# Kernel tuning notes

Hardware: AMD Instinct MI355X
Metric: run time of the kernel (lower is better)

The kernel has to match this reference:

```python
import jax, jax.numpy as jnp
import numpy as np

ANCHOR = 12.0      # anchor (d,h,w) size used for parametrization
NMS_IOU = 0.25     # suppression threshold
TOPK = 2048        # pre-NMS candidate cap (= stop_after), fixed for jit


def setup_inputs() -> dict:
    key = jax.random.key(0)
    k1, k2 = jax.random.split(key)
    bboxes = jax.random.normal(k1, (2, 6, 64, 96, 96), dtype=jnp.float32)
    scores = jax.random.normal(k2, (2, 64, 96, 96), dtype=jnp.float32)
    return {"bboxes": bboxes, "scores": scores}


def _deparametrize(bboxes):
    # bboxes: (B, 6, D, H, W), parametrized as in Ren et al. 2017
    D, H, W = bboxes.shape[2:]
    axes = [jnp.arange(s, dtype=bboxes.dtype) + 0.5 for s in (D, H, W)]
    zyx = jnp.stack(jnp.meshgrid(*axes, indexing='ij'))        # (3, D, H, W)
    abs_zyx = bboxes[:, :3] * ANCHOR + zyx[None]               # center coords
    abs_dhw = jnp.exp(bboxes[:, 3:]) * ANCHOR                  # sizes
    return jnp.concatenate([abs_zyx, abs_dhw], axis=1)


def _pairwise_iou(b1, b2):
    # b1: (N,6), b2: (M,6) with (z,y,x,d,h,w)
    c1, s1 = b1[:, :3], b1[:, 3:]
    c2, s2 = b2[:, :3], b2[:, 3:]
    lo = jnp.maximum((c1 - s1 / 2)[:, None, :], (c2 - s2 / 2)[None, :, :])
    hi = jnp.minimum((c1 + s1 / 2)[:, None, :], (c2 + s2 / 2)[None, :, :])
    inter = jnp.clip(hi - lo, 0).prod(-1)                      # (N, M)
    union = s1.prod(-1)[:, None] + s2.prod(-1)[None, :] - inter
    return inter / union


def _nms_one(boxes_flat, scores_flat):
    # boxes_flat: (P, 6), scores_flat: (P,)
    scores_top, idx = jax.lax.top_k(scores_flat, TOPK)
    boxes_top = boxes_flat[idx]                                # (K, 6)
    ious = _pairwise_iou(boxes_top, boxes_top)                 # (K, K)
    ar = jnp.arange(TOPK)

    def body(keep, i):
        # suppress lower-scored boxes overlapping a kept box i
        suppress = (ious[i] > NMS_IOU) & (ar > i) & keep[i]
        return keep & ~suppress, None

    keep, _ = jax.lax.scan(body, jnp.ones(TOPK, dtype=bool), ar)
    out = jnp.concatenate([scores_top[:, None], boxes_top], axis=1)  # (K, 7)
    return jnp.where(keep[:, None], out, 0.0)


def reference(bboxes, scores):
    abs_boxes = _deparametrize(bboxes)                         # (B, 6, D, H, W)
    B = bboxes.shape[0]
    boxes_flat = abs_boxes.reshape(B, 6, -1).transpose(0, 2, 1)  # (B, P, 6)
    scores_flat = scores.reshape(B, -1)                          # (B, P)
    # (B, TOPK, 7): column 0 = score, columns 1:7 = (z,y,x,d,h,w); suppressed rows zeroed
    return jax.vmap(_nms_one)(boxes_flat, scores_flat)
```

## Files before the change

### kernel.cpp

```cpp
#include <hip/hip_runtime.h>
#include <math.h>

typedef unsigned int U32;
typedef unsigned long long U64;

constexpr int N_SP   = 64 * 96 * 96;
constexpr int NBATCH = 2;
constexpr int K_TOP  = 2048;
constexpr int NBINS  = 8192;
constexpr int CAP    = 8192;
constexpr int CAPB   = 128;
constexpr float ANCHOR_F = 12.0f;
constexpr float NMS_IOU_F = 0.25f;

constexpr size_t OFF_HIST = 0;
constexpr size_t OFF_CNT  = OFF_HIST + 2 * NBINS * 4;
constexpr size_t OFF_THR  = OFF_CNT + 256;
constexpr size_t OFF_RANK = OFF_THR + 256;
constexpr size_t OFF_CAND = OFF_RANK + 2 * CAP * 4;
constexpr size_t OFF_BOX  = OFF_CAND + 2 * CAP * 8;
constexpr size_t OFF_MASK = OFF_BOX + 2 * 14 * K_TOP * 4;
constexpr size_t OFF_DIAG = OFF_MASK + 2 * K_TOP * 64 * 4;
constexpr size_t OFF_BCNT = OFF_DIAG + 2 * K_TOP * 4;
constexpr size_t OFF_BKT  = OFF_BCNT + 512;

__device__ __forceinline__ U32 mono_of(float f) {
  U32 u = __float_as_uint(f);
  return (u & 0x80000000u) ? ~u : (u | 0x80000000u);
}
__device__ __forceinline__ float un_mono(U32 m) {
  U32 u = (m & 0x80000000u) ? (m ^ 0x80000000u) : ~m;
  return __uint_as_float(u);
}

__global__ void __launch_bounds__(256) k_zero(U32* hist, U32* rank, U32* cnt,
                                              U32* bcnt) {
  int g = blockIdx.x * 256 + threadIdx.x;
  hist[g] = 0;
  rank[g] = 0;
  if (g < NBATCH) cnt[g] = 0;
  if (g < 2 * 64) bcnt[g] = 0;
}

__global__ void __launch_bounds__(256) k_hist(const float* __restrict__ scores,
                                              U32* __restrict__ hist) {
  int b = blockIdx.y;
  const float4* s4 = (const float4*)(scores + (size_t)b * N_SP)
                     + (size_t)blockIdx.x * 2048 + threadIdx.x;
  float4 v[8];
#pragma unroll
  for (int e = 0; e < 8; ++e) v[e] = s4[e * 256];
  __shared__ U32 lh[NBINS];
  for (int k = threadIdx.x; k < NBINS; k += 256) lh[k] = 0;
  __syncthreads();
#pragma unroll
  for (int e = 0; e < 8; ++e) {
    atomicAdd(&lh[mono_of(v[e].x) >> 19], 1u);
    atomicAdd(&lh[mono_of(v[e].y) >> 19], 1u);
    atomicAdd(&lh[mono_of(v[e].z) >> 19], 1u);
    atomicAdd(&lh[mono_of(v[e].w) >> 19], 1u);
  }
  __syncthreads();
  U32* gh = hist + (size_t)b * NBINS;
  for (int k = threadIdx.x; k < NBINS; k += 256) {
    U32 c = lh[k];
    if (c) atomicAdd(&gh[k], c);
  }
}

__global__ void __launch_bounds__(256) k_thresh(const U32* __restrict__ hist,
                                                U32* __restrict__ thr) {
  int b = blockIdx.x;
  const U32* h = hist + (size_t)b * NBINS;
  __shared__ U32 part[256];
  int t = threadIdx.x;
  int base = NBINS - 32 * (t + 1);
  U32 s = 0;
  for (int k = 0; k < 32; ++k) s += h[base + k];
  part[t] = s;
  __syncthreads();
  if (t == 0) {
    U32 cum = 0, bin = 0;
    for (int c = 0; c < 256; ++c) {
      U32 p = part[c];
      if (cum + p >= (U32)K_TOP) {
        int hb = NBINS - 32 * c - 1;
        for (int k = 0; k < 32; ++k) {
          cum += h[hb - k];
          if (cum >= (U32)K_TOP) { bin = (U32)(hb - k); break; }
        }
        break;
      }
      cum += p;
    }
    thr[b] = bin;
  }
}

__global__ void __launch_bounds__(256) k_collect(const float* __restrict__ scores,
                                                 const U32* __restrict__ thr,
                                                 U32* __restrict__ cnt,
                                                 U64* __restrict__ cand) {
  int b = blockIdx.y;
  U32 tb = thr[b];
  const float4* s4 = (const float4*)(scores + (size_t)b * N_SP)
                     + (size_t)blockIdx.x * 1024 + threadIdx.x;
  float4 v[4];
#pragma unroll
  for (int e = 0; e < 4; ++e) v[e] = s4[e * 256];
  __shared__ U64 lbuf[4096];
  __shared__ U32 lcnt, lbase;
  if (threadIdx.x == 0) lcnt = 0;
  __syncthreads();
#pragma unroll
  for (int e = 0; e < 4; ++e) {
    U32 i0 = (blockIdx.x * 1024 + e * 256 + threadIdx.x) * 4;
    float vv[4] = {v[e].x, v[e].y, v[e].z, v[e].w};
#pragma unroll
    for (int c = 0; c < 4; ++c) {
      U32 m = mono_of(vv[c]);
      if ((m >> 19) >= tb) {
        U32 p = atomicAdd(&lcnt, 1u);
        lbuf[p] = ((U64)m << 32) | (U32)(~(i0 + c));
      }
    }
  }
  __syncthreads();
  if (threadIdx.x == 0 && lcnt) lbase = atomicAdd(&cnt[b], lcnt);
  __syncthreads();
  U32 n = lcnt;
  if (n == 0) return;
  U32 base = lbase;
  U64* cb = cand + (size_t)b * CAP;
  for (U32 k = threadIdx.x; k < n; k += 256) {
    U32 pos = base + k;
    if (pos < (U32)CAP) cb[pos] = lbuf[k];
  }
}

__global__ void __launch_bounds__(256) k_count(const U64* __restrict__ cand,
                                               const U32* __restrict__ cnt,
                                               U32* __restrict__ rank) {
  int b = blockIdx.y;
  U32 C = cnt[b]; if (C > (U32)CAP) C = CAP;
  U32 g = blockIdx.x * 256 + threadIdx.x;
  U32 t = g & (CAP - 1);
  U32 sgm = g >> 13;
  if (t >= C) return;
  const U64* cb = cand + (size_t)b * CAP;
  U64 key = cb[t];
  U32 segLen = (C + 7) >> 3;
  U32 j0 = sgm * segLen;
  U32 j1 = j0 + segLen; if (j1 > C) j1 = C;
  U32 c = 0;
  for (U32 j = j0; j < j1; ++j) c += (cb[j] > key) ? 1u : 0u;
  if (c) atomicAdd(&rank[(size_t)b * CAP + t], c);
}

#pragma clang fp contract(off)

__global__ void __launch_bounds__(256) k_gather(const float* __restrict__ bboxes,
                                                const U64* __restrict__ cand,
                                                const U32* __restrict__ cnt,
                                                const U32* __restrict__ rank,
                                                float* __restrict__ box) {
  int b = blockIdx.y;
  U32 C = cnt[b]; if (C > (U32)CAP) C = CAP;
  U32 t = blockIdx.x * 256 + threadIdx.x;
  if (t >= C) return;
  U32 r = rank[(size_t)b * CAP + t];
  if (r >= (U32)K_TOP) return;
  U64 key = cand[(size_t)b * CAP + t];
  U32 idx = ~(U32)(key & 0xFFFFFFFFull);
  float sc = un_mono((U32)(key >> 32));
  int d = idx / 9216;
  int rem = idx - d * 9216;
  int h = rem / 96;
  int w = rem - h * 96;
  const float* src = bboxes + (size_t)b * 6 * N_SP + idx;
  float r0 = src[0];
  float r1 = src[(size_t)N_SP];
  float r2 = src[(size_t)2 * N_SP];
  float r3 = src[(size_t)3 * N_SP];
  float r4 = src[(size_t)4 * N_SP];
  float r5 = src[(size_t)5 * N_SP];
  float cz = r0 * ANCHOR_F + ((float)d + 0.5f);
  float cy = r1 * ANCHOR_F + ((float)h + 0.5f);
  float cx = r2 * ANCHOR_F + ((float)w + 0.5f);
  float sz = (float)exp((double)r3) * ANCHOR_F;
  float sy = (float)exp((double)r4) * ANCHOR_F;
  float sx = (float)exp((double)r5) * ANCHOR_F;
  float* B0 = box + (size_t)b * 14 * K_TOP;
  B0[0 * K_TOP + r] = cz;  B0[1 * K_TOP + r] = cy;  B0[2 * K_TOP + r] = cx;
  B0[3 * K_TOP + r] = sz;  B0[4 * K_TOP + r] = sy;  B0[5 * K_TOP + r] = sx;
  B0[6 * K_TOP + r] = cz - sz * 0.5f;
  B0[7 * K_TOP + r] = cy - sy * 0.5f;
  B0[8 * K_TOP + r] = cx - sx * 0.5f;
  B0[9 * K_TOP + r] = cz + sz * 0.5f;
  B0[10 * K_TOP + r] = cy + sy * 0.5f;
  B0[11 * K_TOP + r] = cx + sx * 0.5f;
  B0[12 * K_TOP + r] = (sz * sy) * sx;
  B0[13 * K_TOP + r] = sc;
}

__global__ void __launch_bounds__(256) k_mask(const float* __restrict__ box,
                                              U32* __restrict__ mask,
                                              U32* __restrict__ diag,
                                              U32* __restrict__ bcnt,
                                              U64* __restrict__ bkt) {
  int b = blockIdx.y;
  int it = blockIdx.x >> 2;
  int jq = blockIdx.x & 3;
  const float* B0 = box + (size_t)b * 14 * K_TOP;
  __shared__ float ls[7][512];
  int j0 = jq * 512;
  for (int k = threadIdx.x; k < 7 * 512; k += 256) {
    int a = k >> 9, j = k & 511;
    ls[a][j] = B0[(size_t)(6 + a) * K_TOP + j0 + j];
  }
  __syncthreads();
  int lane = threadIdx.x & 63;
  int wv = threadIdx.x >> 6;
  int i = it * 64 + lane;
  float imin0 = B0[6 * K_TOP + i], imin1 = B0[7 * K_TOP + i], imin2 = B0[8 * K_TOP + i];
  float imax0 = B0[9 * K_TOP + i], imax1 = B0[10 * K_TOP + i], imax2 = B0[11 * K_TOP + i];
  float ivol  = B0[12 * K_TOP + i];
  U32 wbits[4];
  int jb = wv * 128;
#pragma unroll
  for (int wl = 0; wl < 4; ++wl) {
    U32 bits = 0;
    for (int bit = 0; bit < 32; ++bit) {
      int jl = jb + wl * 32 + bit;
      int j = j0 + jl;
      float lo0 = fmaxf(imin0, ls[0][jl]);
      float lo1 = fmaxf(imin1, ls[1][jl]);
      float lo2 = fmaxf(imin2, ls[2][jl]);
      float hi0 = fminf(imax0, ls[3][jl]);
      float hi1 = fminf(imax1, ls[4][jl]);
      float hi2 = fminf(imax2, ls[5][jl]);
      float d0 = fmaxf(hi0 - lo0, 0.0f);
      float d1 = fmaxf(hi1 - lo1, 0.0f);
      float d2 = fmaxf(hi2 - lo2, 0.0f);
      float inter = (d0 * d1) * d2;
      float uni = (ivol + ls[6][jl]) - inter;
      float iou = inter / uni;
      bits |= ((iou > NMS_IOU_F) && (j > i)) ? (1u << bit) : 0u;
    }
    wbits[wl] = bits;
  }
  uint4* mrow = (uint4*)(mask + ((size_t)(b * K_TOP + i)) * 64);
  mrow[jq * 4 + wv] = make_uint4(wbits[0], wbits[1], wbits[2], wbits[3]);
  U32* dgp = diag + (size_t)b * K_TOP;
  int g_src = i >> 5;
  U32* bc = bcnt + b * 64 + g_src;
  U64* bb = bkt + ((size_t)(b * 64 + g_src)) * CAPB;
#pragma unroll
  for (int wl = 0; wl < 4; ++wl) {
    int w = jq * 16 + wv * 4 + wl;
    if (w == (i >> 5)) dgp[i] = wbits[wl];
    if (wbits[wl]) {
      U32 p = atomicAdd(bc, 1u);
      if (p < (U32)CAPB)
        bb[p] = ((U64)((U32)((i & 31) << 6) | (U32)w) << 32) | wbits[wl];
    }
  }
}

__global__ void __launch_bounds__(256) k_nms(const float* __restrict__ box,
                                             const U32* __restrict__ mask,
                                             const U32* __restrict__ diag,
                                             const U32* __restrict__ bcnt,
                                             const U64* __restrict__ bkt,
                                             float* __restrict__ out) {
  int b = blockIdx.x;
  int tid = threadIdx.x;
  int wv = tid >> 6, lane = tid & 63;
  const U32* mk = mask + (size_t)b * K_TOP * 64;
  const U32* dgp = diag + (size_t)b * K_TOP;
  const U32* bcg = bcnt + b * 64;
  const U64* bkg = bkt + (size_t)b * 64 * CAPB;

  __shared__ U32 ldiag[K_TOP];
  __shared__ U64 lbkt[64 * CAPB];
  __shared__ U32 lcnt[64];
  __shared__ U32 keepArr[64];

  for (int k = tid; k < K_TOP; k += 256) ldiag[k] = dgp[k];
  {
    U32 nc[16];
#pragma unroll
    for (int j = 0; j < 16; ++j) nc[j] = bcg[wv * 16 + j];
#pragma unroll
    for (int j = 0; j < 16; ++j) {
      int gg = wv * 16 + j;
      if (lane == 0) lcnt[gg] = nc[j];
      U32 nn = nc[j] > (U32)CAPB ? (U32)CAPB : nc[j];
      for (U32 e = (U32)lane; e < nn; e += 64)
        lbkt[gg * CAPB + e] = bkg[(size_t)gg * CAPB + e];
    }
  }
  __syncthreads();

  if (wv == 0) {
    U32 keep = 0xFFFFFFFFu;
    U32 cnt_l = lcnt[lane];
    bool ovf = (__ballot(cnt_l > (U32)CAPB) != 0ull);
    if (!ovf) {
      for (int g = 0; g < 64; ++g) {
        U32 kw = (U32)__builtin_amdgcn_readlane((int)keep, g);
        if (!kw) continue;
        U32 dgl = ldiag[g * 32 + (lane & 31)];
        U32 nzw = (U32)__ballot(dgl != 0);
        U32 m = kw & nzw;
        while (m) {
          int q = __builtin_ctz(m);
          if ((kw >> q) & 1u)
            kw &= ~(U32)__builtin_amdgcn_readlane((int)dgl, q);
          m &= m - 1;
        }
        U32 n = (U32)__builtin_amdgcn_readlane((int)cnt_l, g);
        U32 acc = 0;
        for (U32 e0 = 0; e0 < n; e0 += 64) {
          U64 ev = lbkt[(U32)g * CAPB + e0 + (U32)lane];
          U32 evLo = (U32)ev, evHi = (U32)(ev >> 32);
          U32 lim = (n - e0 > 64u) ? 64u : (n - e0);
          for (U32 t = 0; t < lim; ++t) {
            U32 hi = (U32)__builtin_amdgcn_readlane((int)evHi, (int)t);
            U32 bt = (U32)__builtin_amdgcn_readlane((int)evLo, (int)t);
            U32 il = (hi >> 6) & 31u, w = hi & 63u;
            if ((kw >> il) & 1u)
              acc |= (w == (U32)lane) ? bt : 0u;
          }
        }
        keep &= ~acc;
      }
    } else {
      for (int g = 0; g < 64; ++g) {
        U32 kw = (U32)__builtin_amdgcn_readlane((int)keep, g);
        U32 dgl = ldiag[g * 32 + (lane & 31)];
#pragma unroll
        for (int q = 0; q < 32; ++q)
          if ((kw >> q) & 1u)
            kw &= ~(U32)__builtin_amdgcn_readlane((int)dgl, q);
        U32 rw[32];
#pragma unroll
        for (int q = 0; q < 32; ++q)
          rw[q] = mk[(size_t)(g * 32 + q) * 64 + lane];
        U32 acc = 0;
#pragma unroll
        for (int q = 0; q < 32; ++q) acc |= ((kw >> q) & 1u) ? rw[q] : 0u;
        keep &= ~acc;
      }
    }
    keepArr[lane] = keep;
  }
  __syncthreads();

  const float* B0 = box + (size_t)b * 14 * K_TOP;
  for (int t = tid; t < K_TOP; t += 256) {
    U32 kp = (keepArr[t >> 5] >> (t & 31)) & 1u;
    float sc = B0[13 * K_TOP + t];
    float vz = B0[0 * K_TOP + t], vy = B0[1 * K_TOP + t], vx = B0[2 * K_TOP + t];
    float dz = B0[3 * K_TOP + t], dy = B0[4 * K_TOP + t], dx = B0[5 * K_TOP + t];
    float* o = out + (size_t)(b * K_TOP + t) * 7;
    o[0] = kp ? sc : 0.0f;
    o[1] = kp ? vz : 0.0f;
    o[2] = kp ? vy : 0.0f;
    o[3] = kp ? vx : 0.0f;
    o[4] = kp ? dz : 0.0f;
    o[5] = kp ? dy : 0.0f;
    o[6] = kp ? dx : 0.0f;
  }
}

extern "C" void kernel_launch(void* const* d_in, const int* in_sizes, int n_in,
                              void* d_out, int out_size, void* d_ws, size_t ws_size,
                              hipStream_t stream) {
  const float* bboxes = (const float*)d_in[0];
  const float* scores = (const float*)d_in[1];
  float* out = (float*)d_out;

  char* ws = (char*)d_ws;
  U32* hist = (U32*)(ws + OFF_HIST);
  U32* cnt  = (U32*)(ws + OFF_CNT);
  U32* thr  = (U32*)(ws + OFF_THR);
  U32* rank = (U32*)(ws + OFF_RANK);
  U64* cand = (U64*)(ws + OFF_CAND);
  float* box = (float*)(ws + OFF_BOX);
  U32* mask = (U32*)(ws + OFF_MASK);
  U32* diag = (U32*)(ws + OFF_DIAG);
  U32* bcnt = (U32*)(ws + OFF_BCNT);
  U64* bkt  = (U64*)(ws + OFF_BKT);

  k_zero<<<64, 256, 0, stream>>>(hist, rank, cnt, bcnt);
  k_hist<<<dim3(72, NBATCH), 256, 0, stream>>>(scores, hist);
  k_thresh<<<NBATCH, 256, 0, stream>>>(hist, thr);
  k_collect<<<dim3(144, NBATCH), 256, 0, stream>>>(scores, thr, cnt, cand);
  k_count<<<dim3(256, NBATCH), 256, 0, stream>>>(cand, cnt, rank);
  k_gather<<<dim3(CAP / 256, NBATCH), 256, 0, stream>>>(bboxes, cand, cnt, rank, box);
  k_mask<<<dim3(128, NBATCH), 256, 0, stream>>>(box, mask, diag, bcnt, bkt);
  k_nms<<<NBATCH, 256, 0, stream>>>(box, mask, diag, bcnt, bkt, out);
}
```

Measured before the change: 182.2 us.

## Fuse all NMS stages into one cooperative persistent kernel with grid syncs

Replaces the eight separate kernel launches with a single cooperative kernel of 256 blocks that runs every stage (zero, histogram, threshold, collect, rank, gather, IoU mask, serial NMS) and separates them with grid-wide syncs. The aim is to remove launch overheads and inter-kernel gaps. In the fused version every block computes the threshold redundantly, and ranking runs in 32 blocks doing full O(C) scans with no atomics or rank buffer. It also halves the per-group bucket capacity, which may route more cases to the slower overflow path, and each grid.sync adds its own cost.

Result: slower. 507.5 us (+178.6%).

```diff
diff --git a/kernel.cpp b/kernel.cpp
--- a/kernel.cpp
+++ b/kernel.cpp
@@ -1,5 +1,8 @@
 #include <hip/hip_runtime.h>
+#include <hip/hip_cooperative_groups.h>
 #include <math.h>
+
+namespace cg = cooperative_groups;
 
 typedef unsigned int U32;
 typedef unsigned long long U64;
@@ -9,15 +12,13 @@
 constexpr int K_TOP  = 2048;
 constexpr int NBINS  = 8192;
 constexpr int CAP    = 8192;
-constexpr int CAPB   = 128;
+constexpr int CAPB   = 64;
 constexpr float ANCHOR_F = 12.0f;
 constexpr float NMS_IOU_F = 0.25f;
 
 constexpr size_t OFF_HIST = 0;
 constexpr size_t OFF_CNT  = OFF_HIST + 2 * NBINS * 4;
-constexpr size_t OFF_THR  = OFF_CNT + 256;
-constexpr size_t OFF_RANK = OFF_THR + 256;
-constexpr size_t OFF_CAND = OFF_RANK + 2 * CAP * 4;
+constexpr size_t OFF_CAND = OFF_CNT + 256;
 constexpr size_t OFF_BOX  = OFF_CAND + 2 * CAP * 8;
 constexpr size_t OFF_MASK = OFF_BOX + 2 * 14 * K_TOP * 4;
 constexpr size_t OFF_DIAG = OFF_MASK + 2 * K_TOP * 64 * 4;
@@ -33,344 +34,332 @@
   return __uint_as_float(u);
 }
 
-__global__ void __launch_bounds__(256) k_zero(U32* hist, U32* rank, U32* cnt,
-                                              U32* bcnt) {
-  int g = blockIdx.x * 256 + threadIdx.x;
-  hist[g] = 0;
-  rank[g] = 0;
-  if (g < NBATCH) cnt[g] = 0;
-  if (g < 2 * 64) bcnt[g] = 0;
-}
-
-__global__ void __launch_bounds__(256) k_hist(const float* __restrict__ scores,
-                                              U32* __restrict__ hist) {
-  int b = blockIdx.y;
-  const float4* s4 = (const float4*)(scores + (size_t)b * N_SP)
-                     + (size_t)blockIdx.x * 2048 + threadIdx.x;
-  float4 v[8];
-#pragma unroll
-  for (int e = 0; e < 8; ++e) v[e] = s4[e * 256];
-  __shared__ U32 lh[NBINS];
-  for (int k = threadIdx.x; k < NBINS; k += 256) lh[k] = 0;
-  __syncthreads();
-#pragma unroll
-  for (int e = 0; e < 8; ++e) {
-    atomicAdd(&lh[mono_of(v[e].x) >> 19], 1u);
-    atomicAdd(&lh[mono_of(v[e].y) >> 19], 1u);
-    atomicAdd(&lh[mono_of(v[e].z) >> 19], 1u);
-    atomicAdd(&lh[mono_of(v[e].w) >> 19], 1u);
-  }
-  __syncthreads();
-  U32* gh = hist + (size_t)b * NBINS;
-  for (int k = threadIdx.x; k < NBINS; k += 256) {
-    U32 c = lh[k];
-    if (c) atomicAdd(&gh[k], c);
-  }
-}
-
-__global__ void __launch_bounds__(256) k_thresh(const U32* __restrict__ hist,
-                                                U32* __restrict__ thr) {
-  int b = blockIdx.x;
-  const U32* h = hist + (size_t)b * NBINS;
-  __shared__ U32 part[256];
-  int t = threadIdx.x;
-  int base = NBINS - 32 * (t + 1);
-  U32 s = 0;
-  for (int k = 0; k < 32; ++k) s += h[base + k];
-  part[t] = s;
-  __syncthreads();
-  if (t == 0) {
-    U32 cum = 0, bin = 0;
-    for (int c = 0; c < 256; ++c) {
-      U32 p = part[c];
-      if (cum + p >= (U32)K_TOP) {
-        int hb = NBINS - 32 * c - 1;
-        for (int k = 0; k < 32; ++k) {
-          cum += h[hb - k];
-          if (cum >= (U32)K_TOP) { bin = (U32)(hb - k); break; }
+#pragma clang fp contract(off)
+
+__global__ void __launch_bounds__(256, 1)
+k_all(const float* __restrict__ bboxes, const float* __restrict__ scores,
+      float* __restrict__ out, char* __restrict__ ws) {
+  cg::grid_group grid = cg::this_grid();
+  const int gid = blockIdx.x;
+  const int tid = threadIdx.x;
+
+  U32* hist = (U32*)(ws + OFF_HIST);
+  U32* cnt  = (U32*)(ws + OFF_CNT);
+  U64* cand = (U64*)(ws + OFF_CAND);
+  float* box = (float*)(ws + OFF_BOX);
+  U32* mask = (U32*)(ws + OFF_MASK);
+  U32* diag = (U32*)(ws + OFF_DIAG);
+  U32* bcnt = (U32*)(ws + OFF_BCNT);
+  U64* bkt  = (U64*)(ws + OFF_BKT);
+
+  __shared__ union SMem {
+    U32 hist[NBINS];
+    struct { U64 lbuf[4096]; U32 lcnt, lbase; } col;
+    U32 part[256];
+    float ls[7][512];
+    struct { U64 lbkt[64 * CAPB]; U32 ldiag[K_TOP];
+             U32 lcnt[64]; U32 keepArr[64]; } nms;
+  } sm;
+  __shared__ U32 sthr[NBATCH];
+
+  {
+    int g = gid * 256 + tid;
+    if (g < 2 * NBINS) hist[g] = 0;
+    if (g < NBATCH) cnt[g] = 0;
+    if (g < 2 * 64) bcnt[g] = 0;
+  }
+  grid.sync();
+
+  if (gid < 144) {
+    int b = gid / 72, wt = gid - b * 72;
+    const float4* s4 = (const float4*)(scores + (size_t)b * N_SP)
+                       + (size_t)wt * 2048 + tid;
+    float4 v[8];
+#pragma unroll
+    for (int e = 0; e < 8; ++e) v[e] = s4[e * 256];
+    for (int k = tid; k < NBINS; k += 256) sm.hist[k] = 0;
+    __syncthreads();
+#pragma unroll
+    for (int e = 0; e < 8; ++e) {
+      atomicAdd(&sm.hist[mono_of(v[e].x) >> 19], 1u);
+      atomicAdd(&sm.hist[mono_of(v[e].y) >> 19], 1u);
+      atomicAdd(&sm.hist[mono_of(v[e].z) >> 19], 1u);
+      atomicAdd(&sm.hist[mono_of(v[e].w) >> 19], 1u);
+    }
+    __syncthreads();
+    U32* gh = hist + (size_t)b * NBINS;
+    for (int k = tid; k < NBINS; k += 256) {
+      U32 c = sm.hist[k];
+      if (c) atomicAdd(&gh[k], c);
+    }
+  }
+  grid.sync();
+
+  for (int bb = 0; bb < NBATCH; ++bb) {
+    const U32* h = hist + (size_t)bb * NBINS;
+    int base = NBINS - 32 * (tid + 1);
+    U32 s = 0;
+    for (int k = 0; k < 32; ++k) s += h[base + k];
+    __syncthreads();
+    sm.part[tid] = s;
+    __syncthreads();
+    if (tid == 0) {
+      U32 cum = 0, bin = 0;
+      for (int c = 0; c < 256; ++c) {
+        U32 p = sm.part[c];
+        if (cum + p >= (U32)K_TOP) {
+          int hb = NBINS - 32 * c - 1;
+          for (int k = 0; k < 32; ++k) {
+            cum += h[hb - k];
+            if (cum >= (U32)K_TOP) { bin = (U32)(hb - k); break; }
+          }
+          break;
         }
-        break;
-      }
-      cum += p;
-    }
-    thr[b] = bin;
-  }
-}
-
-__global__ void __launch_bounds__(256) k_collect(const float* __restrict__ scores,
-                                                 const U32* __restrict__ thr,
-                                                 U32* __restrict__ cnt,
-                                                 U64* __restrict__ cand) {
-  int b = blockIdx.y;
-  U32 tb = thr[b];
-  const float4* s4 = (const float4*)(scores + (size_t)b * N_SP)
-                     + (size_t)blockIdx.x * 1024 + threadIdx.x;
-  float4 v[4];
-#pragma unroll
-  for (int e = 0; e < 4; ++e) v[e] = s4[e * 256];
-  __shared__ U64 lbuf[4096];
-  __shared__ U32 lcnt, lbase;
-  if (threadIdx.x == 0) lcnt = 0;
-  __syncthreads();
-#pragma unroll
-  for (int e = 0; e < 4; ++e) {
-    U32 i0 = (blockIdx.x * 1024 + e * 256 + threadIdx.x) * 4;
-    float vv[4] = {v[e].x, v[e].y, v[e].z, v[e].w};
-#pragma unroll
-    for (int c = 0; c < 4; ++c) {
-      U32 m = mono_of(vv[c]);
-      if ((m >> 19) >= tb) {
-        U32 p = atomicAdd(&lcnt, 1u);
-        lbuf[p] = ((U64)m << 32) | (U32)(~(i0 + c));
-      }
-    }
-  }
-  __syncthreads();
-  if (threadIdx.x == 0 && lcnt) lbase = atomicAdd(&cnt[b], lcnt);
-  __syncthreads();
-  U32 n = lcnt;
-  if (n == 0) return;
-  U32 base = lbase;
-  U64* cb = cand + (size_t)b * CAP;
-  for (U32 k = threadIdx.x; k < n; k += 256) {
-    U32 pos = base + k;
-    if (pos < (U32)CAP) cb[pos] = lbuf[k];
-  }
-}
-
-__global__ void __launch_bounds__(256) k_count(const U64* __restrict__ cand,
-                                               const U32* __restrict__ cnt,
-                                               U32* __restrict__ rank) {
-  int b = blockIdx.y;
-  U32 C = cnt[b]; if (C > (U32)CAP) C = CAP;
-  U32 g = blockIdx.x * 256 + threadIdx.x;
-  U32 t = g & (CAP - 1);
-  U32 sgm = g >> 13;
-  if (t >= C) return;
-  const U64* cb = cand + (size_t)b * CAP;
-  U64 key = cb[t];
-  U32 segLen = (C + 7) >> 3;
-  U32 j0 = sgm * segLen;
-  U32 j1 = j0 + segLen; if (j1 > C) j1 = C;
-  U32 c = 0;
-  for (U32 j = j0; j < j1; ++j) c += (cb[j] > key) ? 1u : 0u;
-  if (c) atomicAdd(&rank[(size_t)b * CAP + t], c);
-}
-
-#pragma clang fp contract(off)
-
-__global__ void __launch_bounds__(256) k_gather(const float* __restrict__ bboxes,
-                                                const U64* __restrict__ cand,
-                                                const U32* __restrict__ cnt,
-                                                const U32* __restrict__ rank,
-                                                float* __restrict__ box) {
-  int b = blockIdx.y;
-  U32 C = cnt[b]; if (C > (U32)CAP) C = CAP;
-  U32 t = blockIdx.x * 256 + threadIdx.x;
-  if (t >= C) return;
-  U32 r = rank[(size_t)b * CAP + t];
-  if (r >= (U32)K_TOP) return;
-  U64 key = cand[(size_t)b * CAP + t];
-  U32 idx = ~(U32)(key & 0xFFFFFFFFull);
-  float sc = un_mono((U32)(key >> 32));
-  int d = idx / 9216;
-  int rem = idx - d * 9216;
-  int h = rem / 96;
-  int w = rem - h * 96;
-  const float* src = bboxes + (size_t)b * 6 * N_SP + idx;
-  float r0 = src[0];
-  float r1 = src[(size_t)N_SP];
-  float r2 = src[(size_t)2 * N_SP];
-  float r3 = src[(size_t)3 * N_SP];
-  float r4 = src[(size_t)4 * N_SP];
-  float r5 = src[(size_t)5 * N_SP];
-  float cz = r0 * ANCHOR_F + ((float)d + 0.5f);
-  float cy = r1 * ANCHOR_F + ((float)h + 0.5f);
-  float cx = r2 * ANCHOR_F + ((float)w + 0.5f);
-  float sz = (float)exp((double)r3) * ANCHOR_F;
-  float sy = (float)exp((double)r4) * ANCHOR_F;
-  float sx = (float)exp((double)r5) * ANCHOR_F;
-  float* B0 = box + (size_t)b * 14 * K_TOP;
-  B0[0 * K_TOP + r] = cz;  B0[1 * K_TOP + r] = cy;  B0[2 * K_TOP + r] = cx;
-  B0[3 * K_TOP + r] = sz;  B0[4 * K_TOP + r] = sy;  B0[5 * K_TOP + r] = sx;
-  B0[6 * K_TOP + r] = cz - sz * 0.5f;
-  B0[7 * K_TOP + r] = cy - sy * 0.5f;
-  B0[8 * K_TOP + r] = cx - sx * 0.5f;
-  B0[9 * K_TOP + r] = cz + sz * 0.5f;
-  B0[10 * K_TOP + r] = cy + sy * 0.5f;
-  B0[11 * K_TOP + r] = cx + sx * 0.5f;
-  B0[12 * K_TOP + r] = (sz * sy) * sx;
-  B0[13 * K_TOP + r] = sc;
-}
-
-__global__ void __launch_bounds__(256) k_mask(const float* __restrict__ box,
-                                              U32* __restrict__ mask,
-                                              U32* __restrict__ diag,
-                                              U32* __restrict__ bcnt,
-                                              U64* __restrict__ bkt) {
-  int b = blockIdx.y;
-  int it = blockIdx.x >> 2;
-  int jq = blockIdx.x & 3;
-  const float* B0 = box + (size_t)b * 14 * K_TOP;
-  __shared__ float ls[7][512];
-  int j0 = jq * 512;
-  for (int k = threadIdx.x; k < 7 * 512; k += 256) {
-    int a = k >> 9, j = k & 511;
-    ls[a][j] = B0[(size_t)(6 + a) * K_TOP + j0 + j];
-  }
-  __syncthreads();
-  int lane = threadIdx.x & 63;
-  int wv = threadIdx.x >> 6;
-  int i = it * 64 + lane;
-  float imin0 = B0[6 * K_TOP + i], imin1 = B0[7 * K_TOP + i], imin2 = B0[8 * K_TOP + i];
-  float imax0 = B0[9 * K_TOP + i], imax1 = B0[10 * K_TOP + i], imax2 = B0[11 * K_TOP + i];
-  float ivol  = B0[12 * K_TOP + i];
-  U32 wbits[4];
-  int jb = wv * 128;
-#pragma unroll
-  for (int wl = 0; wl < 4; ++wl) {
-    U32 bits = 0;
-    for (int bit = 0; bit < 32; ++bit) {
-      int jl = jb + wl * 32 + bit;
-      int j = j0 + jl;
-      float lo0 = fmaxf(imin0, ls[0][jl]);
-      float lo1 = fmaxf(imin1, ls[1][jl]);
-      float lo2 = fmaxf(imin2, ls[2][jl]);
-      float hi0 = fminf(imax0, ls[3][jl]);
-      float hi1 = fminf(imax1, ls[4][jl]);
-      float hi2 = fminf(imax2, ls[5][jl]);
-      float d0 = fmaxf(hi0 - lo0, 0.0f);
-      float d1 = fmaxf(hi1 - lo1, 0.0f);
-      float d2 = fmaxf(hi2 - lo2, 0.0f);
-      float inter = (d0 * d1) * d2;
-      float uni = (ivol + ls[6][jl]) - inter;
-      float iou = inter / uni;
-      bits |= ((iou > NMS_IOU_F) && (j > i)) ? (1u << bit) : 0u;
-    }
-    wbits[wl] = bits;
-  }
-  uint4* mrow = (uint4*)(mask + ((size_t)(b * K_TOP + i)) * 64);
-  mrow[jq * 4 + wv] = make_uint4(wbits[0], wbits[1], wbits[2], wbits[3]);
-  U32* dgp = diag + (size_t)b * K_TOP;
-  int g_src = i >> 5;
-  U32* bc = bcnt + b * 64 + g_src;
-  U64* bb = bkt + ((size_t)(b * 64 + g_src)) * CAPB;
-#pragma unroll
-  for (int wl = 0; wl < 4; ++wl) {
-    int w = jq * 16 + wv * 4 + wl;
-    if (w == (i >> 5)) dgp[i] = wbits[wl];
-    if (wbits[wl]) {
-      U32 p = atomicAdd(bc, 1u);
-      if (p < (U32)CAPB)
-        bb[p] = ((U64)((U32)((i & 31) << 6) | (U32)w) << 32) | wbits[wl];
-    }
-  }
-}
-
-__global__ void __launch_bounds__(256) k_nms(const float* __restrict__ box,
-                                             const U32* __restrict__ mask,
-                                             const U32* __restrict__ diag,
-                                             const U32* __restrict__ bcnt,
-                                             const U64* __restrict__ bkt,
-                                             float* __restrict__ out) {
-  int b = blockIdx.x;
-  int tid = threadIdx.x;
-  int wv = tid >> 6, lane = tid & 63;
-  const U32* mk = mask + (size_t)b * K_TOP * 64;
-  const U32* dgp = diag + (size_t)b * K_TOP;
-  const U32* bcg = bcnt + b * 64;
-  const U64* bkg = bkt + (size_t)b * 64 * CAPB;
-
-  __shared__ U32 ldiag[K_TOP];
-  __shared__ U64 lbkt[64 * CAPB];
-  __shared__ U32 lcnt[64];
-  __shared__ U32 keepArr[64];
-
-  for (int k = tid; k < K_TOP; k += 256) ldiag[k] = dgp[k];
+        cum += p;
+      }
+      sthr[bb] = bin;
+    }
+    __syncthreads();
+  }
+
+  for (int vb = gid; vb < 288; vb += 256) {
+    int b = vb / 144, wt = vb - b * 144;
+    U32 tb = sthr[b];
+    const float4* s4 = (const float4*)(scores + (size_t)b * N_SP)
+                       + (size_t)wt * 1024 + tid;
+    float4 v[4];
+#pragma unroll
+    for (int e = 0; e < 4; ++e) v[e] = s4[e * 256];
+    if (tid == 0) sm.col.lcnt = 0;
+    __syncthreads();
+#pragma unroll
+    for (int e = 0; e < 4; ++e) {
+      U32 i0 = (wt * 1024 + e * 256 + tid) * 4;
+      float vv[4] = {v[e].x, v[e].y, v[e].z, v[e].w};
+#pragma unroll
+      for (int c = 0; c < 4; ++c) {
+        U32 m = mono_of(vv[c]);
+        if ((m >> 19) >= tb) {
+          U32 p = atomicAdd(&sm.col.lcnt, 1u);
+          sm.col.lbuf[p] = ((U64)m << 32) | (U32)(~(i0 + c));
+        }
+      }
+    }
+    __syncthreads();
+    if (tid == 0 && sm.col.lcnt) sm.col.lbase = atomicAdd(&cnt[b], sm.col.lcnt);
+    __syncthreads();
+    U32 n = sm.col.lcnt;
+    if (n) {
+      U32 base = sm.col.lbase;
+      U64* cb = cand + (size_t)b * CAP;
+      for (U32 k = tid; k < n; k += 256) {
+        U32 pos = base + k;
+        if (pos < (U32)CAP) cb[pos] = sm.col.lbuf[k];
+      }
+    }
+    __syncthreads();
+  }
+  grid.sync();
+
+  if (gid < 32) {
+    int b = gid >> 4, blk = gid & 15;
+    U32 C = cnt[b]; if (C > (U32)CAP) C = CAP;
+    const U64* cb = cand + (size_t)b * CAP;
+    U32 t0 = (U32)(blk * 512 + tid), t1 = t0 + 256;
+    U64 k0 = (t0 < C) ? cb[t0] : 0ull;
+    U64 k1 = (t1 < C) ? cb[t1] : 0ull;
+    U32 rk0 = 0, rk1 = 0;
+    for (U32 j = 0; j < C; ++j) {
+      U64 kj = cb[j];
+      rk0 += (kj > k0) ? 1u : 0u;
+      rk1 += (kj > k1) ? 1u : 0u;
+    }
+#pragma unroll
+    for (int s = 0; s < 2; ++s) {
+      U32 t = s ? t1 : t0;
+      U64 key = s ? k1 : k0;
+      U32 r = s ? rk1 : rk0;
+      if (t >= C || r >= (U32)K_TOP) continue;
+      U32 idx = ~(U32)(key & 0xFFFFFFFFull);
+      float sc = un_mono((U32)(key >> 32));
+      int d = idx / 9216;
+      int rem = idx - d * 9216;
+      int h = rem / 96;
+      int w = rem - h * 96;
+      const float* src = bboxes + (size_t)b * 6 * N_SP + idx;
+      float r0 = src[0];
+      float r1 = src[(size_t)N_SP];
+      float r2 = src[(size_t)2 * N_SP];
+      float r3 = src[(size_t)3 * N_SP];
+      float r4 = src[(size_t)4 * N_SP];
+      float r5 = src[(size_t)5 * N_SP];
+      float cz = r0 * ANCHOR_F + ((float)d + 0.5f);
+      float cy = r1 * ANCHOR_F + ((float)h + 0.5f);
+      float cx = r2 * ANCHOR_F + ((float)w + 0.5f);
+      float sz = (float)exp((double)r3) * ANCHOR_F;
+      float sy = (float)exp((double)r4) * ANCHOR_F;
+      float sx = (float)exp((double)r5) * ANCHOR_F;
+      float* B0 = box + (size_t)b * 14 * K_TOP;
+      B0[0 * K_TOP + r] = cz;  B0[1 * K_TOP + r] = cy;  B0[2 * K_TOP + r] = cx;
+      B0[3 * K_TOP + r] = sz;  B0[4 * K_TOP + r] = sy;  B0[5 * K_TOP + r] = sx;
+      B0[6 * K_TOP + r] = cz - sz * 0.5f;
+      B0[7 * K_TOP + r] = cy - sy * 0.5f;
+      B0[8 * K_TOP + r] = cx - sx * 0.5f;
+      B0[9 * K_TOP + r] = cz + sz * 0.5f;
+      B0[10 * K_TOP + r] = cy + sy * 0.5f;
+      B0[11 * K_TOP + r] = cx + sx * 0.5f;
+      B0[12 * K_TOP + r] = (sz * sy) * sx;
+      B0[13 * K_TOP + r] = sc;
+    }
+  }
+  grid.sync();
+
   {
-    U32 nc[16];
-#pragma unroll
-    for (int j = 0; j < 16; ++j) nc[j] = bcg[wv * 16 + j];
-#pragma unroll
-    for (int j = 0; j < 16; ++j) {
-      int gg = wv * 16 + j;
-      if (lane == 0) lcnt[gg] = nc[j];
-      U32 nn = nc[j] > (U32)CAPB ? (U32)CAPB : nc[j];
-      for (U32 e = (U32)lane; e < nn; e += 64)
-        lbkt[gg * CAPB + e] = bkg[(size_t)gg * CAPB + e];
-    }
-  }
-  __syncthreads();
-
-  if (wv == 0) {
-    U32 keep = 0xFFFFFFFFu;
-    U32 cnt_l = lcnt[lane];
-    bool ovf = (__ballot(cnt_l > (U32)CAPB) != 0ull);
-    if (!ovf) {
-      for (int g = 0; g < 64; ++g) {
-        U32 kw = (U32)__builtin_amdgcn_readlane((int)keep, g);
-        if (!kw) continue;
-        U32 dgl = ldiag[g * 32 + (lane & 31)];
-        U32 nzw = (U32)__ballot(dgl != 0);
-        U32 m = kw & nzw;
-        while (m) {
-          int q = __builtin_ctz(m);
-          if ((kw >> q) & 1u)
-            kw &= ~(U32)__builtin_amdgcn_readlane((int)dgl, q);
-          m &= m - 1;
+    int b = gid >> 7;
+    int x = gid & 127;
+    int it = x >> 2;
+    int jq = x & 3;
+    const float* B0 = box + (size_t)b * 14 * K_TOP;
+    int j0 = jq * 512;
+    __syncthreads();
+    for (int k = tid; k < 7 * 512; k += 256) {
+      int a = k >> 9, j = k & 511;
+      sm.ls[a][j] = B0[(size_t)(6 + a) * K_TOP + j0 + j];
+    }
+    __syncthreads();
+    int lane = tid & 63;
+    int wv = tid >> 6;
+    int i = it * 64 + lane;
+    float imin0 = B0[6 * K_TOP + i], imin1 = B0[7 * K_TOP + i], imin2 = B0[8 * K_TOP + i];
+    float imax0 = B0[9 * K_TOP + i], imax1 = B0[10 * K_TOP + i], imax2 = B0[11 * K_TOP + i];
+    float ivol  = B0[12 * K_TOP + i];
+    U32 wbits[4];
+    int jb = wv * 128;
+#pragma unroll
+    for (int wl = 0; wl < 4; ++wl) {
+      U32 bits = 0;
+      for (int bit = 0; bit < 32; ++bit) {
+        int jl = jb + wl * 32 + bit;
+        int j = j0 + jl;
+        float lo0 = fmaxf(imin0, sm.ls[0][jl]);
+        float lo1 = fmaxf(imin1, sm.ls[1][jl]);
+        float lo2 = fmaxf(imin2, sm.ls[2][jl]);
+        float hi0 = fminf(imax0, sm.ls[3][jl]);
+        float hi1 = fminf(imax1, sm.ls[4][jl]);
+        float hi2 = fminf(imax2, sm.ls[5][jl]);
+        float d0 = fmaxf(hi0 - lo0, 0.0f);
+        float d1 = fmaxf(hi1 - lo1, 0.0f);
+        float d2 = fmaxf(hi2 - lo2, 0.0f);
+        float inter = (d0 * d1) * d2;
+        float uni = (ivol + sm.ls[6][jl]) - inter;
+        float iou = inter / uni;
+        bits |= ((iou > NMS_IOU_F) && (j > i)) ? (1u << bit) : 0u;
+      }
+      wbits[wl] = bits;
+    }
+    uint4* mrow = (uint4*)(mask + ((size_t)(b * K_TOP + i)) * 64);
+    mrow[jq * 4 + wv] = make_uint4(wbits[0], wbits[1], wbits[2], wbits[3]);
+    U32* dgp = diag + (size_t)b * K_TOP;
+    int g_src = i >> 5;
+    U32* bc = bcnt + b * 64 + g_src;
+    U64* bb = bkt + ((size_t)(b * 64 + g_src)) * CAPB;
+#pragma unroll
+    for (int wl = 0; wl < 4; ++wl) {
+      int w = jq * 16 + wv * 4 + wl;
+      if (w == (i >> 5)) dgp[i] = wbits[wl];
+      if (wbits[wl]) {
+        U32 p = atomicAdd(bc, 1u);
+        if (p < (U32)CAPB)
+          bb[p] = ((U64)((U32)((i & 31) << 6) | (U32)w) << 32) | wbits[wl];
+      }
+    }
+  }
+  grid.sync();
+
+  if (gid < NBATCH) {
+    int b = gid;
+    int wv = tid >> 6, lane = tid & 63;
+    const U32* mk = mask + (size_t)b * K_TOP * 64;
+    const U32* dgp = diag + (size_t)b * K_TOP;
+    const U32* bcg = bcnt + b * 64;
+    const U64* bkg = bkt + (size_t)b * 64 * CAPB;
+
+    __syncthreads();
+    for (int k = tid; k < K_TOP; k += 256) sm.nms.ldiag[k] = dgp[k];
+    for (int k = tid; k < 64 * CAPB; k += 256) sm.nms.lbkt[k] = bkg[k];
+    if (tid < 64) sm.nms.lcnt[tid] = bcg[tid];
+    __syncthreads();
+
+    if (wv == 0) {
+      U32 keep = 0xFFFFFFFFu;
+      U32 cnt_l = sm.nms.lcnt[lane];
+      bool ovf = (__ballot(cnt_l > (U32)CAPB) != 0ull);
+      if (!ovf) {
+        for (int g = 0; g < 64; ++g) {
+          U32 kw = (U32)__builtin_amdgcn_readlane((int)keep, g);
+          if (!kw) continue;
+          U32 dgl = sm.nms.ldiag[g * 32 + (lane & 31)];
+          U32 nzw = (U32)__ballot(dgl != 0);
+          U32 m = kw & nzw;
+          while (m) {
+            int q = __builtin_ctz(m);
+            if ((kw >> q) & 1u)
+              kw &= ~(U32)__builtin_amdgcn_readlane((int)dgl, q);
+            m &= m - 1;
+          }
+          U32 n = (U32)__builtin_amdgcn_readlane((int)cnt_l, g);
+          U32 acc = 0;
+          for (U32 e0 = 0; e0 < n; e0 += 64) {
+            U64 ev = sm.nms.lbkt[(U32)g * CAPB + e0 + (U32)lane];
+            U32 evLo = (U32)ev, evHi = (U32)(ev >> 32);
+            U32 lim = (n - e0 > 64u) ? 64u : (n - e0);
+            for (U32 t = 0; t < lim; ++t) {
+              U32 hi = (U32)__builtin_amdgcn_readlane((int)evHi, (int)t);
+              U32 bt = (U32)__builtin_amdgcn_readlane((int)evLo, (int)t);
+              U32 il = (hi >> 6) & 31u, w = hi & 63u;
+              if ((kw >> il) & 1u)
+                acc |= (w == (U32)lane) ? bt : 0u;
+            }
+          }
+          keep &= ~acc;
         }
-        U32 n = (U32)__builtin_amdgcn_readlane((int)cnt_l, g);
-        U32 acc = 0;
-        for (U32 e0 = 0; e0 < n; e0 += 64) {
-          U64 ev = lbkt[(U32)g * CAPB + e0 + (U32)lane];
-          U32 evLo = (U32)ev, evHi = (U32)(ev >> 32);
-          U32 lim = (n - e0 > 64u) ? 64u : (n - e0);
-          for (U32 t = 0; t < lim; ++t) {
-            U32 hi = (U32)__builtin_amdgcn_readlane((int)evHi, (int)t);
-            U32 bt = (U32)__builtin_amdgcn_readlane((int)evLo, (int)t);
-            U32 il = (hi >> 6) & 31u, w = hi & 63u;
-            if ((kw >> il) & 1u)
-              acc |= (w == (U32)lane) ? bt : 0u;
-          }
+      } else {
+        for (int g = 0; g < 64; ++g) {
+          U32 kw = (U32)__builtin_amdgcn_readlane((int)keep, g);
+          U32 dgl = sm.nms.ldiag[g * 32 + (lane & 31)];
+#pragma unroll
+          for (int q = 0; q < 32; ++q)
+            if ((kw >> q) & 1u)
+              kw &= ~(U32)__builtin_amdgcn_readlane((int)dgl, q);
+          U32 rw[32];
+#pragma unroll
+          for (int q = 0; q < 32; ++q)
+            rw[q] = mk[(size_t)(g * 32 + q) * 64 + lane];
+          U32 acc = 0;
+#pragma unroll
+          for (int q = 0; q < 32; ++q) acc |= ((kw >> q) & 1u) ? rw[q] : 0u;
+          keep &= ~acc;
         }
-        keep &= ~acc;
-      }
-    } else {
-      for (int g = 0; g < 64; ++g) {
-        U32 kw = (U32)__builtin_amdgcn_readlane((int)keep, g);
-        U32 dgl = ldiag[g * 32 + (lane & 31)];
-#pragma unroll
-        for (int q = 0; q < 32; ++q)
-          if ((kw >> q) & 1u)
-            kw &= ~(U32)__builtin_amdgcn_readlane((int)dgl, q);
-        U32 rw[32];
-#pragma unroll
-        for (int q = 0; q < 32; ++q)
-          rw[q] = mk[(size_t)(g * 32 + q) * 64 + lane];
-        U32 acc = 0;
-#pragma unroll
-        for (int q = 0; q < 32; ++q) acc |= ((kw >> q) & 1u) ? rw[q] : 0u;
-        keep &= ~acc;
-      }
-    }
-    keepArr[lane] = keep;
-  }
-  __syncthreads();
-
-  const float* B0 = box + (size_t)b * 14 * K_TOP;
-  for (int t = tid; t < K_TOP; t += 256) {
-    U32 kp = (keepArr[t >> 5] >> (t & 31)) & 1u;
-    float sc = B0[13 * K_TOP + t];
-    float vz = B0[0 * K_TOP + t], vy = B0[1 * K_TOP + t], vx = B0[2 * K_TOP + t];
-    float dz = B0[3 * K_TOP + t], dy = B0[4 * K_TOP + t], dx = B0[5 * K_TOP + t];
-    float* o = out + (size_t)(b * K_TOP + t) * 7;
-    o[0] = kp ? sc : 0.0f;
-    o[1] = kp ? vz : 0.0f;
-    o[2] = kp ? vy : 0.0f;
-    o[3] = kp ? vx : 0.0f;
-    o[4] = kp ? dz : 0.0f;
-    o[5] = kp ? dy : 0.0f;
-    o[6] = kp ? dx : 0.0f;
+      }
+      sm.nms.keepArr[lane] = keep;
+    }
+    __syncthreads();
+
+    const float* B0 = box + (size_t)b * 14 * K_TOP;
+    for (int t = tid; t < K_TOP; t += 256) {
+      U32 kp = (sm.nms.keepArr[t >> 5] >> (t & 31)) & 1u;
+      float sc = B0[13 * K_TOP + t];
+      float vz = B0[0 * K_TOP + t], vy = B0[1 * K_TOP + t], vx = B0[2 * K_TOP + t];
+      float dz = B0[3 * K_TOP + t], dy = B0[4 * K_TOP + t], dx = B0[5 * K_TOP + t];
+      float* o = out + (size_t)(b * K_TOP + t) * 7;
+      o[0] = kp ? sc : 0.0f;
+      o[1] = kp ? vz : 0.0f;
+      o[2] = kp ? vy : 0.0f;
+      o[3] = kp ? vx : 0.0f;
+      o[4] = kp ? dz : 0.0f;
+      o[5] = kp ? dy : 0.0f;
+      o[6] = kp ? dx : 0.0f;
+    }
   }
 }
 
@@ -380,25 +369,9 @@
   const float* bboxes = (const float*)d_in[0];
   const float* scores = (const float*)d_in[1];
   float* out = (float*)d_out;
-
   char* ws = (char*)d_ws;
-  U32* hist = (U32*)(ws + OFF_HIST);
-  U32* cnt  = (U32*)(ws + OFF_CNT);
-  U32* thr  = (U32*)(ws + OFF_THR);
-  U32* rank = (U32*)(ws + OFF_RANK);
-  U64* cand = (U64*)(ws + OFF_CAND);
-  float* box = (float*)(ws + OFF_BOX);
-  U32* mask = (U32*)(ws + OFF_MASK);
-  U32* diag = (U32*)(ws + OFF_DIAG);
-  U32* bcnt = (U32*)(ws + OFF_BCNT);
-  U64* bkt  = (U64*)(ws + OFF_BKT);
-
-  k_zero<<<64, 256, 0, stream>>>(hist, rank, cnt, bcnt);
-  k_hist<<<dim3(72, NBATCH), 256, 0, stream>>>(scores, hist);
-  k_thresh<<<NBATCH, 256, 0, stream>>>(hist, thr);
-  k_collect<<<dim3(144, NBATCH), 256, 0, stream>>>(scores, thr, cnt, cand);
-  k_count<<<dim3(256, NBATCH), 256, 0, stream>>>(cand, cnt, rank);
-  k_gather<<<dim3(CAP / 256, NBATCH), 256, 0, stream>>>(bboxes, cand, cnt, rank, box);
-  k_mask<<<dim3(128, NBATCH), 256, 0, stream>>>(box, mask, diag, bcnt, bkt);
-  k_nms<<<NBATCH, 256, 0, stream>>>(box, mask, diag, bcnt, bkt, out);
+
+  void* args[] = {(void*)&bboxes, (void*)&scores, (void*)&out, (void*)&ws};
+  hipLaunchCooperativeKernel((const void*)k_all, dim3(256), dim3(256), args, 0,
+                             stream);
 }
```

## Fuse threshold into collect, merge rank count with gather, shrink bucket cap

Applied to the files above, without the earlier changes.

The threshold search now runs redundantly inside every collect block, which removes the separate k_thresh launch. The rank counting and the box gather are merged into one kernel. Each thread ranks two candidates by a full scan over all C, so no rank buffer, atomics or zeroing are needed. The NMS bucket capacity drops from 128 to 64 and the bucket load becomes a plain copy. This cuts three launches, but the rank loop is now serial per thread over up to 8192 keys with only 32 blocks, and more buckets may overflow and fall back to a slow path.

Result: slower. 308.9 us (+69.6%).

```diff
diff --git a/kernel.cpp b/kernel.cpp
--- a/kernel.cpp
+++ b/kernel.cpp
@@ -9,15 +9,13 @@
 constexpr int K_TOP  = 2048;
 constexpr int NBINS  = 8192;
 constexpr int CAP    = 8192;
-constexpr int CAPB   = 128;
+constexpr int CAPB   = 64;
 constexpr float ANCHOR_F = 12.0f;
 constexpr float NMS_IOU_F = 0.25f;
 
 constexpr size_t OFF_HIST = 0;
 constexpr size_t OFF_CNT  = OFF_HIST + 2 * NBINS * 4;
-constexpr size_t OFF_THR  = OFF_CNT + 256;
-constexpr size_t OFF_RANK = OFF_THR + 256;
-constexpr size_t OFF_CAND = OFF_RANK + 2 * CAP * 4;
+constexpr size_t OFF_CAND = OFF_CNT + 256;
 constexpr size_t OFF_BOX  = OFF_CAND + 2 * CAP * 8;
 constexpr size_t OFF_MASK = OFF_BOX + 2 * 14 * K_TOP * 4;
 constexpr size_t OFF_DIAG = OFF_MASK + 2 * K_TOP * 64 * 4;
@@ -33,11 +31,9 @@
   return __uint_as_float(u);
 }
 
-__global__ void __launch_bounds__(256) k_zero(U32* hist, U32* rank, U32* cnt,
-                                              U32* bcnt) {
+__global__ void __launch_bounds__(256) k_zero(U32* hist, U32* cnt, U32* bcnt) {
   int g = blockIdx.x * 256 + threadIdx.x;
   hist[g] = 0;
-  rank[g] = 0;
   if (g < NBATCH) cnt[g] = 0;
   if (g < 2 * 64) bcnt[g] = 0;
 }
@@ -68,18 +64,29 @@
   }
 }
 
-__global__ void __launch_bounds__(256) k_thresh(const U32* __restrict__ hist,
-                                                U32* __restrict__ thr) {
-  int b = blockIdx.x;
+__global__ void __launch_bounds__(256) k_collect(const float* __restrict__ scores,
+                                                 const U32* __restrict__ hist,
+                                                 U32* __restrict__ cnt,
+                                                 U64* __restrict__ cand) {
+  int b = blockIdx.y;
+  int tid = threadIdx.x;
+  const float4* s4 = (const float4*)(scores + (size_t)b * N_SP)
+                     + (size_t)blockIdx.x * 1024 + tid;
+  float4 v[4];
+#pragma unroll
+  for (int e = 0; e < 4; ++e) v[e] = s4[e * 256];
+
+  __shared__ U32 part[256];
+  __shared__ U32 sthr;
   const U32* h = hist + (size_t)b * NBINS;
-  __shared__ U32 part[256];
-  int t = threadIdx.x;
-  int base = NBINS - 32 * (t + 1);
-  U32 s = 0;
-  for (int k = 0; k < 32; ++k) s += h[base + k];
-  part[t] = s;
-  __syncthreads();
-  if (t == 0) {
+  {
+    int base = NBINS - 32 * (tid + 1);
+    U32 s = 0;
+    for (int k = 0; k < 32; ++k) s += h[base + k];
+    part[tid] = s;
+  }
+  __syncthreads();
+  if (tid == 0) {
     U32 cum = 0, bin = 0;
     for (int c = 0; c < 256; ++c) {
       U32 p = part[c];
@@ -93,28 +100,18 @@
       }
       cum += p;
     }
-    thr[b] = bin;
-  }
-}
-
-__global__ void __launch_bounds__(256) k_collect(const float* __restrict__ scores,
-                                                 const U32* __restrict__ thr,
-                                                 U32* __restrict__ cnt,
-                                                 U64* __restrict__ cand) {
-  int b = blockIdx.y;
-  U32 tb = thr[b];
-  const float4* s4 = (const float4*)(scores + (size_t)b * N_SP)
-                     + (size_t)blockIdx.x * 1024 + threadIdx.x;
-  float4 v[4];
-#pragma unroll
-  for (int e = 0; e < 4; ++e) v[e] = s4[e * 256];
+    sthr = bin;
+  }
+  __syncthreads();
+  U32 tb = sthr;
+
   __shared__ U64 lbuf[4096];
   __shared__ U32 lcnt, lbase;
-  if (threadIdx.x == 0) lcnt = 0;
+  if (tid == 0) lcnt = 0;
   __syncthreads();
 #pragma unroll
   for (int e = 0; e < 4; ++e) {
-    U32 i0 = (blockIdx.x * 1024 + e * 256 + threadIdx.x) * 4;
+    U32 i0 = (blockIdx.x * 1024 + e * 256 + tid) * 4;
     float vv[4] = {v[e].x, v[e].y, v[e].z, v[e].w};
 #pragma unroll
     for (int c = 0; c < 4; ++c) {
@@ -126,81 +123,74 @@
     }
   }
   __syncthreads();
-  if (threadIdx.x == 0 && lcnt) lbase = atomicAdd(&cnt[b], lcnt);
+  if (tid == 0 && lcnt) lbase = atomicAdd(&cnt[b], lcnt);
   __syncthreads();
   U32 n = lcnt;
   if (n == 0) return;
   U32 base = lbase;
   U64* cb = cand + (size_t)b * CAP;
-  for (U32 k = threadIdx.x; k < n; k += 256) {
+  for (U32 k = tid; k < n; k += 256) {
     U32 pos = base + k;
     if (pos < (U32)CAP) cb[pos] = lbuf[k];
   }
 }
 
-__global__ void __launch_bounds__(256) k_count(const U64* __restrict__ cand,
-                                               const U32* __restrict__ cnt,
-                                               U32* __restrict__ rank) {
-  int b = blockIdx.y;
+#pragma clang fp contract(off)
+
+__global__ void __launch_bounds__(256) k_cg(const float* __restrict__ bboxes,
+                                            const U64* __restrict__ cand,
+                                            const U32* __restrict__ cnt,
+                                            float* __restrict__ box) {
+  int b = blockIdx.y, blk = blockIdx.x;
+  int tid = threadIdx.x;
   U32 C = cnt[b]; if (C > (U32)CAP) C = CAP;
-  U32 g = blockIdx.x * 256 + threadIdx.x;
-  U32 t = g & (CAP - 1);
-  U32 sgm = g >> 13;
-  if (t >= C) return;
   const U64* cb = cand + (size_t)b * CAP;
-  U64 key = cb[t];
-  U32 segLen = (C + 7) >> 3;
-  U32 j0 = sgm * segLen;
-  U32 j1 = j0 + segLen; if (j1 > C) j1 = C;
-  U32 c = 0;
-  for (U32 j = j0; j < j1; ++j) c += (cb[j] > key) ? 1u : 0u;
-  if (c) atomicAdd(&rank[(size_t)b * CAP + t], c);
-}
-
-#pragma clang fp contract(off)
-
-__global__ void __launch_bounds__(256) k_gather(const float* __restrict__ bboxes,
-                                                const U64* __restrict__ cand,
-                                                const U32* __restrict__ cnt,
-                                                const U32* __restrict__ rank,
-                                                float* __restrict__ box) {
-  int b = blockIdx.y;
-  U32 C = cnt[b]; if (C > (U32)CAP) C = CAP;
-  U32 t = blockIdx.x * 256 + threadIdx.x;
-  if (t >= C) return;
-  U32 r = rank[(size_t)b * CAP + t];
-  if (r >= (U32)K_TOP) return;
-  U64 key = cand[(size_t)b * CAP + t];
-  U32 idx = ~(U32)(key & 0xFFFFFFFFull);
-  float sc = un_mono((U32)(key >> 32));
-  int d = idx / 9216;
-  int rem = idx - d * 9216;
-  int h = rem / 96;
-  int w = rem - h * 96;
-  const float* src = bboxes + (size_t)b * 6 * N_SP + idx;
-  float r0 = src[0];
-  float r1 = src[(size_t)N_SP];
-  float r2 = src[(size_t)2 * N_SP];
-  float r3 = src[(size_t)3 * N_SP];
-  float r4 = src[(size_t)4 * N_SP];
-  float r5 = src[(size_t)5 * N_SP];
-  float cz = r0 * ANCHOR_F + ((float)d + 0.5f);
-  float cy = r1 * ANCHOR_F + ((float)h + 0.5f);
-  float cx = r2 * ANCHOR_F + ((float)w + 0.5f);
-  float sz = (float)exp((double)r3) * ANCHOR_F;
-  float sy = (float)exp((double)r4) * ANCHOR_F;
-  float sx = (float)exp((double)r5) * ANCHOR_F;
-  float* B0 = box + (size_t)b * 14 * K_TOP;
-  B0[0 * K_TOP + r] = cz;  B0[1 * K_TOP + r] = cy;  B0[2 * K_TOP + r] = cx;
-  B0[3 * K_TOP + r] = sz;  B0[4 * K_TOP + r] = sy;  B0[5 * K_TOP + r] = sx;
-  B0[6 * K_TOP + r] = cz - sz * 0.5f;
-  B0[7 * K_TOP + r] = cy - sy * 0.5f;
-  B0[8 * K_TOP + r] = cx - sx * 0.5f;
-  B0[9 * K_TOP + r] = cz + sz * 0.5f;
-  B0[10 * K_TOP + r] = cy + sy * 0.5f;
-  B0[11 * K_TOP + r] = cx + sx * 0.5f;
-  B0[12 * K_TOP + r] = (sz * sy) * sx;
-  B0[13 * K_TOP + r] = sc;
+  U32 t0 = (U32)(blk * 512 + tid), t1 = t0 + 256;
+  U64 k0 = (t0 < C) ? cb[t0] : 0ull;
+  U64 k1 = (t1 < C) ? cb[t1] : 0ull;
+  U32 rk0 = 0, rk1 = 0;
+  for (U32 j = 0; j < C; ++j) {
+    U64 kj = cb[j];
+    rk0 += (kj > k0) ? 1u : 0u;
+    rk1 += (kj > k1) ? 1u : 0u;
+  }
+#pragma unroll
+  for (int s = 0; s < 2; ++s) {
+    U32 t = s ? t1 : t0;
+    U64 key = s ? k1 : k0;
+    U32 r = s ? rk1 : rk0;
+    if (t >= C || r >= (U32)K_TOP) continue;
+    U32 idx = ~(U32)(key & 0xFFFFFFFFull);
+    float sc = un_mono((U32)(key >> 32));
+    int d = idx / 9216;
+    int rem = idx - d * 9216;
+    int h = rem / 96;
+    int w = rem - h * 96;
+    const float* src = bboxes + (size_t)b * 6 * N_SP + idx;
+    float r0 = src[0];
+    float r1 = src[(size_t)N_SP];
+    float r2 = src[(size_t)2 * N_SP];
+    float r3 = src[(size_t)3 * N_SP];
+    float r4 = src[(size_t)4 * N_SP];
+    float r5 = src[(size_t)5 * N_SP];
+    float cz = r0 * ANCHOR_F + ((float)d + 0.5f);
+    float cy = r1 * ANCHOR_F + ((float)h + 0.5f);
+    float cx = r2 * ANCHOR_F + ((float)w + 0.5f);
+    float sz = (float)exp((double)r3) * ANCHOR_F;
+    float sy = (float)exp((double)r4) * ANCHOR_F;
+    float sx = (float)exp((double)r5) * ANCHOR_F;
+    float* B0 = box + (size_t)b * 14 * K_TOP;
+    B0[0 * K_TOP + r] = cz;  B0[1 * K_TOP + r] = cy;  B0[2 * K_TOP + r] = cx;
+    B0[3 * K_TOP + r] = sz;  B0[4 * K_TOP + r] = sy;  B0[5 * K_TOP + r] = sx;
+    B0[6 * K_TOP + r] = cz - sz * 0.5f;
+    B0[7 * K_TOP + r] = cy - sy * 0.5f;
+    B0[8 * K_TOP + r] = cx - sx * 0.5f;
+    B0[9 * K_TOP + r] = cz + sz * 0.5f;
+    B0[10 * K_TOP + r] = cy + sy * 0.5f;
+    B0[11 * K_TOP + r] = cx + sx * 0.5f;
+    B0[12 * K_TOP + r] = (sz * sy) * sx;
+    B0[13 * K_TOP + r] = sc;
+  }
 }
 
 __global__ void __launch_bounds__(256) k_mask(const float* __restrict__ box,
@@ -281,25 +271,14 @@
   const U32* bcg = bcnt + b * 64;
   const U64* bkg = bkt + (size_t)b * 64 * CAPB;
 
+  __shared__ U64 lbkt[64 * CAPB];
   __shared__ U32 ldiag[K_TOP];
-  __shared__ U64 lbkt[64 * CAPB];
   __shared__ U32 lcnt[64];
   __shared__ U32 keepArr[64];
 
   for (int k = tid; k < K_TOP; k += 256) ldiag[k] = dgp[k];
-  {
-    U32 nc[16];
-#pragma unroll
-    for (int j = 0; j < 16; ++j) nc[j] = bcg[wv * 16 + j];
-#pragma unroll
-    for (int j = 0; j < 16; ++j) {
-      int gg = wv * 16 + j;
-      if (lane == 0) lcnt[gg] = nc[j];
-      U32 nn = nc[j] > (U32)CAPB ? (U32)CAPB : nc[j];
-      for (U32 e = (U32)lane; e < nn; e += 64)
-        lbkt[gg * CAPB + e] = bkg[(size_t)gg * CAPB + e];
-    }
-  }
+  for (int k = tid; k < 64 * CAPB; k += 256) lbkt[k] = bkg[k];
+  if (tid < 64) lcnt[tid] = bcg[tid];
   __syncthreads();
 
   if (wv == 0) {
@@ -384,8 +363,6 @@
   char* ws = (char*)d_ws;
   U32* hist = (U32*)(ws + OFF_HIST);
   U32* cnt  = (U32*)(ws + OFF_CNT);
-  U32* thr  = (U32*)(ws + OFF_THR);
-  U32* rank = (U32*)(ws + OFF_RANK);
   U64* cand = (U64*)(ws + OFF_CAND);
   float* box = (float*)(ws + OFF_BOX);
   U32* mask = (U32*)(ws + OFF_MASK);
@@ -393,12 +370,10 @@
   U32* bcnt = (U32*)(ws + OFF_BCNT);
   U64* bkt  = (U64*)(ws + OFF_BKT);
 
-  k_zero<<<64, 256, 0, stream>>>(hist, rank, cnt, bcnt);
+  k_zero<<<64, 256, 0, stream>>>(hist, cnt, bcnt);
   k_hist<<<dim3(72, NBATCH), 256, 0, stream>>>(scores, hist);
-  k_thresh<<<NBATCH, 256, 0, stream>>>(hist, thr);
-  k_collect<<<dim3(144, NBATCH), 256, 0, stream>>>(scores, thr, cnt, cand);
-  k_count<<<dim3(256, NBATCH), 256, 0, stream>>>(cand, cnt, rank);
-  k_gather<<<dim3(CAP / 256, NBATCH), 256, 0, stream>>>(bboxes, cand, cnt, rank, box);
+  k_collect<<<dim3(144, NBATCH), 256, 0, stream>>>(scores, hist, cnt, cand);
+  k_cg<<<dim3(16, NBATCH), 256, 0, stream>>>(bboxes, cand, cnt, box);
   k_mask<<<dim3(128, NBATCH), 256, 0, stream>>>(box, mask, diag, bcnt, bkt);
   k_nms<<<NBATCH, 256, 0, stream>>>(box, mask, diag, bcnt, bkt, out);
 }
```
